# Kernel optimization log

Measured on AMD Instinct MI355X. Metric: run time of the kernel, lower is better.

## Reference

```python
import jax, jax.numpy as jnp
import numpy as np

P_SIZE = 5
NUM_HEAD = 8
GN_EPS = 1e-5
LRELU_SLOPE = 0.2


def conv1x1(w, x, b=None):
    # w: [out_c, in_c], x: [n, in_c, h, w]
    y = jnp.einsum('oc,nchw->nohw', w, x)
    if b is not None:
        y = y + b[None, :, None, None]
    return y


def bilinear_sample(feat, sx, sy):
    """grid_sample(mode='bilinear', padding_mode='zeros', align_corners=True).
    With align_corners=True the normalize/denormalize round-trip in
    deformation_grid/grid_sample is the identity, so sx,sy are raw pixel coords.
    feat: [n,c,H,W]; sx,sy: [n,P,H,W] -> out [n,c,P,H,W]."""
    n, c, H, W = feat.shape
    x0 = jnp.floor(sx)
    y0 = jnp.floor(sy)
    x1 = x0 + 1.0
    y1 = y0 + 1.0
    wx1 = sx - x0
    wx0 = 1.0 - wx1
    wy1 = sy - y0
    wy0 = 1.0 - wy1
    feat_flat = feat.reshape(n, c, H * W)

    def corner(xi, yi, wgt):
        valid = (xi >= 0) & (xi <= W - 1) & (yi >= 0) & (yi <= H - 1)
        xc = jnp.clip(xi, 0, W - 1).astype(jnp.int32)
        yc = jnp.clip(yi, 0, H - 1).astype(jnp.int32)
        idx = (yc * W + xc).reshape(n, -1)                      # [n, P*H*W]
        g = jnp.take_along_axis(feat_flat, idx[:, None, :], axis=2)  # [n,c,P*H*W]
        g = g.reshape(n, c, xi.shape[1], H, W)                  # [n,c,P,H,W]
        wm = (wgt * valid.astype(feat.dtype))[:, None]          # [n,1,P,H,W]
        return g * wm

    return (corner(x0, y0, wx0 * wy0) + corner(x1, y0, wx1 * wy0)
            + corner(x0, y1, wx0 * wy1) + corner(x1, y1, wx1 * wy1))


def sample_coords(deform_field, p_size):
    # deform_field: [n,2,h,w] -> absolute pixel coords sx, sy: [n, p^2, h, w]
    n, _, h, w = deform_field.shape
    padding = (p_size - 1) // 2
    shift = jnp.arange(p_size, dtype=deform_field.dtype) - padding
    shift_y, shift_x = jnp.meshgrid(shift, shift, indexing='ij')  # [p,p]
    shift_y = shift_y.reshape(-1, 1, 1)  # [p^2,1,1]
    shift_x = shift_x.reshape(-1, 1, 1)
    gy = jnp.arange(h, dtype=deform_field.dtype)[:, None]  # [h,1]
    gx = jnp.arange(w, dtype=deform_field.dtype)[None, :]  # [1,w]
    sx = gx[None] + shift_x + deform_field[:, None, 0]     # [n,p^2,h,w]
    sy = gy[None] + shift_y + deform_field[:, None, 1]
    return sx, sy


def setup_inputs() -> dict:
    key = jax.random.key(0)
    ks = jax.random.split(key, 12)
    n, c, h, w = 2, 128, 96, 96
    hid = 256
    s = 0.05
    return {
        'query': jax.random.normal(ks[0], (n, c, h, w), jnp.float32),
        'key': jax.random.normal(ks[1], (n, c, h, w), jnp.float32),
        'value': jax.random.normal(ks[2], (n, c, h, w), jnp.float32),
        'deform_field': jax.random.normal(ks[3], (n, 2, h, w), jnp.float32) * 2.0,
        'w_q': jax.random.normal(ks[4], (c, c), jnp.float32) * s,
        'w_k': jax.random.normal(ks[5], (c, c), jnp.float32) * s,
        'w_v': jax.random.normal(ks[6], (c, c), jnp.float32) * s,
        'w_fc': jax.random.normal(ks[7], (c, c), jnp.float32) * s,
        'mlp_w1': jax.random.normal(ks[8], (hid, c), jnp.float32) * s,
        'mlp_b1': jnp.zeros((hid,), jnp.float32),
        'mlp_w2': jax.random.normal(ks[9], (c, hid), jnp.float32) * s,
        'mlp_b2': jnp.zeros((c,), jnp.float32),
        'gn_gamma': jnp.ones((c,), jnp.float32),
        'gn_beta': jnp.zeros((c,), jnp.float32),
    }


def reference(query, key, value, deform_field, w_q, w_k, w_v, w_fc,
              mlp_w1, mlp_b1, mlp_w2, mlp_b2, gn_gamma, gn_beta):
    p2 = P_SIZE * P_SIZE
    n, c, h, w = query.shape
    d_k = c // NUM_HEAD

    q = conv1x1(w_q, query)   # [n,c,h,w]
    k = conv1x1(w_k, key)
    v = conv1x1(w_v, value)

    # deformable window sampling of keys/values
    sx, sy = sample_coords(deform_field, P_SIZE)      # [n,p^2,h,w]
    k_s = bilinear_sample(k, sx, sy)                  # [n,c,p^2,h,w]
    v_s = bilinear_sample(v, sx, sy)

    # split heads
    q = q.reshape(n, NUM_HEAD, d_k, h, w)
    k_s = k_s.reshape(n, NUM_HEAD, d_k, p2, h, w)
    v_s = v_s.reshape(n, NUM_HEAD, d_k, p2, h, w)

    scale = 1.0 / jnp.sqrt(jnp.asarray(d_k, q.dtype))
    attn = jnp.einsum('nedyx,nedpyx->neyxp', q * scale, k_s)   # [n,head,h,w,p^2]
    attn = jax.nn.softmax(attn, axis=-1)
    out = jnp.einsum('neyxp,nedpyx->nedyx', attn, v_s)          # [n,head,d_v,h,w]
    out = out.reshape(n, c, h, w)
    out = conv1x1(w_fc, out)

    # conv-MLP residual
    hdn = conv1x1(mlp_w1, out, mlp_b1)
    hdn = jnp.where(hdn >= 0, hdn, LRELU_SLOPE * hdn)
    out = out + conv1x1(mlp_w2, hdn, mlp_b2)

    # GroupNorm(1, feat_dim): normalize over (C,H,W) per sample, per-channel affine
    mean = jnp.mean(out, axis=(1, 2, 3), keepdims=True)
    var = jnp.mean(jnp.square(out - mean), axis=(1, 2, 3), keepdims=True)
    out = (out - mean) * jax.lax.rsqrt(var + GN_EPS)
    out = out * gn_gamma[None, :, None, None] + gn_beta[None, :, None, None]
    return out
```

## Files before the change

kernel.cpp:

```cpp
#include <hip/hip_runtime.h>
#include <cstddef>

constexpr int Cc = 128;
constexpr int Hh = 96;
constexpr int Ww = 96;
constexpr int HW = Hh * Ww;
constexpr int Nn = 2;

typedef __attribute__((ext_vector_type(2))) _Float16 f16x2;
typedef __attribute__((ext_vector_type(4))) _Float16 f16x4;
typedef __attribute__((ext_vector_type(8))) _Float16 f16x8;
typedef __attribute__((ext_vector_type(4))) float f32x4;

__device__ __forceinline__ float fdot2(f16x2 a, f16x2 b, float c) {
#if defined(__has_builtin) && __has_builtin(__builtin_amdgcn_fdot2)
    return __builtin_amdgcn_fdot2(a, b, c, false);
#else
    return (float)a[0] * (float)b[0] + (float)a[1] * (float)b[1] + c;
#endif
}

__global__ void __launch_bounds__(256)
wcvt_k(const float* __restrict__ wq, const float* __restrict__ wk,
       const float* __restrict__ wv, const float* __restrict__ wfc,
       const float* __restrict__ w1, const float* __restrict__ w2,
       _Float16* __restrict__ dst)
{
    const int h0 = (blockIdx.x * 256 + threadIdx.x) * 8;
    const float* src; int off, K;
    if (h0 < 16384)      { src = wq;  off = h0;          K = 128; }
    else if (h0 < 32768) { src = wk;  off = h0 - 16384;  K = 128; }
    else if (h0 < 49152) { src = wv;  off = h0 - 32768;  K = 128; }
    else if (h0 < 65536) { src = wfc; off = h0 - 49152;  K = 128; }
    else if (h0 < 98304) { src = w1;  off = h0 - 65536;  K = 128; }
    else                 { src = w2;  off = h0 - 98304;  K = 256; }
    const int fid  = off >> 3;
    const int lane = fid & 63;
    const int n16  = lane & 15, quad = lane >> 4;
    const int t2   = fid >> 6;
    const int kcN  = K / 32;
    const int kc   = t2 % kcN;
    const int mt   = t2 / kcN;
    const int row  = mt * 16 + n16;
    const int col  = kc * 32 + quad * 8;
    const float* s = src + (size_t)row * K + col;
    const float4 a = *(const float4*)s;
    const float4 b = *(const float4*)(s + 4);
    f16x8 h = {(_Float16)a.x, (_Float16)a.y, (_Float16)a.z, (_Float16)a.w,
               (_Float16)b.x, (_Float16)b.y, (_Float16)b.z, (_Float16)b.w};
    *(f16x8*)&dst[h0] = h;
}

__global__ void __launch_bounds__(128)
kv_k(const float* __restrict__ Xk, const float* __restrict__ Xv,
     const _Float16* __restrict__ w16,
     _Float16* __restrict__ k16, _Float16* __restrict__ v16)
{
    const int t  = blockIdx.y;
    const int p0 = blockIdx.x * 64;
    const int z  = blockIdx.z;
    const float* X = (t == 0) ? Xk : Xv;
    _Float16* Y    = (t == 0) ? k16 : v16;
    const _Float16* W = w16 + 16384 + (size_t)t * 16384;

    __shared__ _Float16 xl[128][72];
    const int tid = threadIdx.x;
    {
        const int px4 = (tid & 15) * 4, kg = tid >> 4;
        const float* Xz = X + (size_t)z * Cc * HW + p0 + px4;
#pragma unroll
        for (int kk = 0; kk < 16; ++kk) {
            const int k = kk * 8 + kg;
            float4 a = *(const float4*)&Xz[(size_t)k * HW];
            f16x4 h = {(_Float16)a.x, (_Float16)a.y, (_Float16)a.z, (_Float16)a.w};
            *(f16x4*)&xl[k][px4] = h;
        }
    }
    __syncthreads();

    const int w = tid >> 6, lane = tid & 63;
    const int n16 = lane & 15, quad = lane >> 4;
    const int pw = w * 32;

    f16x8 A[2][4];
#pragma unroll
    for (int mi = 0; mi < 2; ++mi) {
        const int px = pw + mi * 16 + n16;
#pragma unroll
        for (int kcid = 0; kcid < 4; ++kcid) {
            f16x8 av;
#pragma unroll
            for (int j = 0; j < 8; ++j) av[j] = xl[kcid * 32 + quad * 8 + j][px];
            A[mi][kcid] = av;
        }
    }

#pragma unroll
    for (int half = 0; half < 2; ++half) {
        const int oc0 = half * 64;
        f32x4 acc[2][4];
#pragma unroll
        for (int mi = 0; mi < 2; ++mi)
#pragma unroll
            for (int ni = 0; ni < 4; ++ni) acc[mi][ni] = (f32x4)0.f;

#pragma unroll
        for (int kcid = 0; kcid < 4; ++kcid) {
            f16x8 B[4];
#pragma unroll
            for (int ni = 0; ni < 4; ++ni)
                B[ni] = *(const f16x8*)&W[(((half * 4 + ni) * 4 + kcid) * 64 + lane) * 8];
#pragma unroll
            for (int mi = 0; mi < 2; ++mi)
#pragma unroll
                for (int ni = 0; ni < 4; ++ni)
                    acc[mi][ni] = __builtin_amdgcn_mfma_f32_16x16x32_f16(
                        A[mi][kcid], B[ni], acc[mi][ni], 0, 0, 0);
        }

#pragma unroll
        for (int mi = 0; mi < 2; ++mi)
#pragma unroll
            for (int r = 0; r < 4; ++r) {
                const int pix = p0 + pw + mi * 16 + quad * 4 + r;
                const size_t base = ((size_t)z * HW + pix) * Cc + oc0;
#pragma unroll
                for (int ni = 0; ni < 4; ++ni)
                    Y[base + ni * 16 + n16] = (_Float16)acc[mi][ni][r];
            }
    }
}

__global__ void __launch_bounds__(512)
qaf_k(const float* __restrict__ Xq, const _Float16* __restrict__ w16,
      const _Float16* __restrict__ k16, const _Float16* __restrict__ v16,
      const float* __restrict__ df, const float* __restrict__ b1,
      const float* __restrict__ b2, _Float16* __restrict__ y2,
      float* __restrict__ pb)
{
    __shared__ __align__(16) _Float16 xl[128][40];
    __shared__ __align__(16) _Float16 ql[32][136];
    __shared__ __align__(16) _Float16 y1l[32][136];
    __shared__ __align__(16) _Float16 hl[32][264];
    __shared__ float red[16];

    const int z  = blockIdx.z;
    const int bx = blockIdx.x;
    const int ti = (bx & 7) * 36 + (bx >> 3);
    const int p0 = ti * 32;
    const int tid = threadIdx.x, w = tid >> 6, lane = tid & 63;
    const int n16 = lane & 15, quad = lane >> 4;

    {
        const int px4 = (tid & 7) * 4, k0 = tid >> 3;
        const float* Xz = Xq + (size_t)z * Cc * HW + p0 + px4;
#pragma unroll
        for (int kk = 0; kk < 2; ++kk) {
            const int k = kk * 64 + k0;
            float4 a = *(const float4*)&Xz[(size_t)k * HW];
            f16x4 h4 = {(_Float16)a.x, (_Float16)a.y, (_Float16)a.z, (_Float16)a.w};
            *(f16x4*)&xl[k][px4] = h4;
        }
    }
    __syncthreads();

    {
        f32x4 qa[2];
        qa[0] = (f32x4)0.f; qa[1] = (f32x4)0.f;
#pragma unroll
        for (int kc = 0; kc < 4; ++kc) {
            f16x8 A[2];
#pragma unroll
            for (int mi = 0; mi < 2; ++mi) {
                f16x8 av;
#pragma unroll
                for (int j = 0; j < 8; ++j)
                    av[j] = xl[kc * 32 + quad * 8 + j][mi * 16 + n16];
                A[mi] = av;
            }
            const f16x8 B = *(const f16x8*)&w16[((w * 4 + kc) * 64 + lane) * 8];
#pragma unroll
            for (int mi = 0; mi < 2; ++mi)
                qa[mi] = __builtin_amdgcn_mfma_f32_16x16x32_f16(A[mi], B, qa[mi], 0, 0, 0);
        }
#pragma unroll
        for (int mi = 0; mi < 2; ++mi)
#pragma unroll
            for (int r = 0; r < 4; ++r)
                ql[mi * 16 + quad * 4 + r][w * 16 + n16] = (_Float16)qa[mi][r];
    }
    __syncthreads();

    {
        const int lpx = w * 4 + (lane >> 4);
        const int pix = p0 + lpx;
        const int y = pix / Ww, x = pix - y * Ww;
        const int co = n16 * 8;

        const float dx = df[((size_t)z * 2 + 0) * HW + pix];
        const float dy = df[((size_t)z * 2 + 1) * HW + pix];
        const float flx = floorf(dx), fly = floorf(dy);
        const int bxp = x - 2 + (int)flx;
        const int byp = y - 2 + (int)fly;
        const float wx1 = dx - flx, wx0 = 1.f - wx1;
        const float wy1 = dy - fly, wy0 = 1.f - wy1;
        const float s00 = wy0 * wx0 * 0.25f, s01 = wy0 * wx1 * 0.25f,
                    s10 = wy1 * wx0 * 0.25f, s11 = wy1 * wx1 * 0.25f;

        const f16x8 qv8 = *(const f16x8*)&ql[lpx][co];
        const f16x2 q0 = {qv8[0], qv8[1]}, q1 = {qv8[2], qv8[3]},
                    q2 = {qv8[4], qv8[5]}, q3 = {qv8[6], qv8[7]};

        const _Float16* kp = k16 + ((size_t)z * HW) * Cc + co;
        const _Float16* vp = v16 + ((size_t)z * HW) * Cc + co;

        const bool inb = (bxp >= 0) & (byp >= 0) & (bxp <= Ww - 6) & (byp <= Hh - 6);
        const int allin = __all(inb);

        float qk[36];
        if (allin) {
            const _Float16* kr = kp + (size_t)(byp * Ww + bxp) * Cc;
#pragma unroll
            for (int r = 0; r < 6; ++r) {
#pragma unroll
                for (int c = 0; c < 6; ++c) {
                    const f16x8 kv = *(const f16x8*)&kr[c * Cc];
                    f16x2 k0 = {kv[0], kv[1]}, k1 = {kv[2], kv[3]};
                    f16x2 k2 = {kv[4], kv[5]}, k3 = {kv[6], kv[7]};
                    float d = fdot2(q0, k0, 0.f);
                    d = fdot2(q1, k1, d);
                    d = fdot2(q2, k2, d);
                    d = fdot2(q3, k3, d);
                    qk[r * 6 + c] = d;
                }
                kr += Ww * Cc;
            }
        } else {
#pragma unroll
            for (int r = 0; r < 6; ++r) {
                const int yr = byp + r;
                const bool rv = (yr >= 0) & (yr < Hh);
                const int yc = min(max(yr, 0), Hh - 1);
                const _Float16* kr = kp + (size_t)(yc * Ww) * Cc;
#pragma unroll
                for (int c = 0; c < 6; ++c) {
                    const int xc = bxp + c;
                    const bool cv = rv & (xc >= 0) & (xc < Ww);
                    const int xcc = min(max(xc, 0), Ww - 1);
                    const f16x8 kv = *(const f16x8*)&kr[xcc * Cc];
                    f16x2 k0 = {kv[0], kv[1]}, k1 = {kv[2], kv[3]};
                    f16x2 k2 = {kv[4], kv[5]}, k3 = {kv[6], kv[7]};
                    float d = fdot2(q0, k0, 0.f);
                    d = fdot2(q1, k1, d);
                    d = fdot2(q2, k2, d);
                    d = fdot2(q3, k3, d);
                    qk[r * 6 + c] = cv ? d : 0.f;
                }
            }
        }

        float a[25];
#pragma unroll
        for (int py = 0; py < 5; ++py)
#pragma unroll
            for (int px = 0; px < 5; ++px) {
                float tv = s00 * qk[py * 6 + px];
                tv = fmaf(s01, qk[py * 6 + px + 1], tv);
                tv = fmaf(s10, qk[(py + 1) * 6 + px], tv);
                tv = fmaf(s11, qk[(py + 1) * 6 + px + 1], tv);
                a[py * 5 + px] = tv;
            }
#pragma unroll
        for (int i = 0; i < 25; ++i) a[i] += __shfl_xor(a[i], 1, 64);

        float mx = a[0];
#pragma unroll
        for (int i = 1; i < 25; ++i) mx = fmaxf(mx, a[i]);
        float ssum = 0.f;
#pragma unroll
        for (int i = 0; i < 25; ++i) { a[i] = __expf(a[i] - mx); ssum += a[i]; }
        const float inv = 1.f / ssum;

        float tmp[6][5];
#pragma unroll
        for (int r = 0; r < 6; ++r)
#pragma unroll
            for (int px = 0; px < 5; ++px) {
                float tv = 0.f;
                if (r < 5)  tv = a[r * 5 + px] * wy0;
                if (r >= 1) tv = fmaf(a[(r - 1) * 5 + px], wy1, tv);
                tmp[r][px] = tv;
            }
        float wsum[36];
#pragma unroll
        for (int r = 0; r < 6; ++r)
#pragma unroll
            for (int c = 0; c < 6; ++c) {
                float tv = 0.f;
                if (c < 5)  tv = tmp[r][c] * wx0;
                if (c >= 1) tv = fmaf(tmp[r][c - 1], wx1, tv);
                wsum[r * 6 + c] = tv;
            }

        float o[8] = {0.f, 0.f, 0.f, 0.f, 0.f, 0.f, 0.f, 0.f};
        if (allin) {
            const _Float16* vr = vp + (size_t)(byp * Ww + bxp) * Cc;
#pragma unroll
            for (int r = 0; r < 6; ++r) {
#pragma unroll
                for (int c = 0; c < 6; ++c) {
                    const f16x8 vv = *(const f16x8*)&vr[c * Cc];
                    const float wgt = wsum[r * 6 + c];
#pragma unroll
                    for (int j = 0; j < 8; ++j)
                        o[j] = fmaf(wgt, (float)vv[j], o[j]);
                }
                vr += Ww * Cc;
            }
        } else {
#pragma unroll
            for (int r = 0; r < 6; ++r) {
                const int yr = byp + r;
                const bool rv = (yr >= 0) & (yr < Hh);
                const int yc = min(max(yr, 0), Hh - 1);
                const _Float16* vr = vp + (size_t)(yc * Ww) * Cc;
#pragma unroll
                for (int c = 0; c < 6; ++c) {
                    const int xc = bxp + c;
                    const bool cv = rv & (xc >= 0) & (xc < Ww);
                    const int xcc = min(max(xc, 0), Ww - 1);
                    const f16x8 vv = *(const f16x8*)&vr[xcc * Cc];
                    const float wgt = cv ? wsum[r * 6 + c] : 0.f;
#pragma unroll
                    for (int j = 0; j < 8; ++j)
                        o[j] = fmaf(wgt, (float)vv[j], o[j]);
                }
            }
        }

        f16x8 ov;
#pragma unroll
        for (int j = 0; j < 8; ++j) ov[j] = (_Float16)(o[j] * inv);
        *(f16x8*)&ql[lpx][co] = ov;
    }
    __syncthreads();

    const _Float16* Wfc = w16 + 49152;
    const _Float16* W1  = w16 + 65536;
    const _Float16* W2  = w16 + 98304;

    f32x4 acc1[2];
    acc1[0] = (f32x4)0.f; acc1[1] = (f32x4)0.f;
#pragma unroll
    for (int kc = 0; kc < 4; ++kc) {
        f16x8 A[2];
#pragma unroll
        for (int mi = 0; mi < 2; ++mi)
            A[mi] = *(const f16x8*)&ql[mi * 16 + n16][kc * 32 + quad * 8];
        const f16x8 B = *(const f16x8*)&Wfc[((w * 4 + kc) * 64 + lane) * 8];
#pragma unroll
        for (int mi = 0; mi < 2; ++mi)
            acc1[mi] = __builtin_amdgcn_mfma_f32_16x16x32_f16(A[mi], B, acc1[mi], 0, 0, 0);
    }
#pragma unroll
    for (int mi = 0; mi < 2; ++mi)
#pragma unroll
        for (int r = 0; r < 4; ++r)
            y1l[mi * 16 + quad * 4 + r][w * 16 + n16] = (_Float16)acc1[mi][r];
    __syncthreads();

    {
        f32x4 acc2[2][2];
#pragma unroll
        for (int mi = 0; mi < 2; ++mi)
#pragma unroll
            for (int ni = 0; ni < 2; ++ni) acc2[mi][ni] = (f32x4)0.f;
#pragma unroll
        for (int kc = 0; kc < 4; ++kc) {
            f16x8 A[2];
#pragma unroll
            for (int mi = 0; mi < 2; ++mi)
                A[mi] = *(const f16x8*)&y1l[mi * 16 + n16][kc * 32 + quad * 8];
#pragma unroll
            for (int ni = 0; ni < 2; ++ni) {
                const f16x8 B = *(const f16x8*)&W1[(((w * 2 + ni) * 4 + kc) * 64 + lane) * 8];
#pragma unroll
                for (int mi = 0; mi < 2; ++mi)
                    acc2[mi][ni] = __builtin_amdgcn_mfma_f32_16x16x32_f16(
                        A[mi], B, acc2[mi][ni], 0, 0, 0);
            }
        }
        float b1v[2];
#pragma unroll
        for (int ni = 0; ni < 2; ++ni) b1v[ni] = b1[w * 32 + ni * 16 + n16];
#pragma unroll
        for (int mi = 0; mi < 2; ++mi)
#pragma unroll
            for (int ni = 0; ni < 2; ++ni)
#pragma unroll
                for (int r = 0; r < 4; ++r) {
                    float tv = acc2[mi][ni][r] + b1v[ni];
                    tv = tv >= 0.f ? tv : 0.2f * tv;
                    hl[mi * 16 + quad * 4 + r][w * 32 + ni * 16 + n16] = (_Float16)tv;
                }
    }
    __syncthreads();

    f32x4 acc3[2];
    acc3[0] = (f32x4)0.f; acc3[1] = (f32x4)0.f;
#pragma unroll
    for (int kc = 0; kc < 8; ++kc) {
        f16x8 A[2];
#pragma unroll
        for (int mi = 0; mi < 2; ++mi)
            A[mi] = *(const f16x8*)&hl[mi * 16 + n16][kc * 32 + quad * 8];
        const f16x8 B = *(const f16x8*)&W2[((w * 8 + kc) * 64 + lane) * 8];
#pragma unroll
        for (int mi = 0; mi < 2; ++mi)
            acc3[mi] = __builtin_amdgcn_mfma_f32_16x16x32_f16(A[mi], B, acc3[mi], 0, 0, 0);
    }

    const float b2v = b2[w * 16 + n16];
    float lsum = 0.f, lsq = 0.f;
#pragma unroll
    for (int mi = 0; mi < 2; ++mi)
#pragma unroll
        for (int r = 0; r < 4; ++r) {
            const int pix = p0 + mi * 16 + quad * 4 + r;
            const float tv = acc3[mi][r] + b2v + acc1[mi][r];
            lsum += tv; lsq += tv * tv;
            y2[((size_t)z * HW + pix) * Cc + w * 16 + n16] = (_Float16)tv;
        }

#pragma unroll
    for (int m = 1; m < 64; m <<= 1) {
        lsum += __shfl_xor(lsum, m, 64);
        lsq  += __shfl_xor(lsq,  m, 64);
    }
    if (lane == 0) { red[w * 2] = lsum; red[w * 2 + 1] = lsq; }
    __syncthreads();
    if (tid == 0) {
        float S = 0.f, Q = 0.f;
#pragma unroll
        for (int i = 0; i < 8; ++i) { S += red[i * 2]; Q += red[i * 2 + 1]; }
        const int bid = z * (HW / 32) + bx;
        pb[bid * 2 + 0] = S;
        pb[bid * 2 + 1] = Q;
    }
}

__global__ void __launch_bounds__(256)
gn_k(const _Float16* __restrict__ y2, const float* __restrict__ pb,
     const float* __restrict__ gamma, const float* __restrict__ beta,
     float* __restrict__ out, const int nPerZ)
{
    __shared__ float t[32][68];
    __shared__ float redm[8];
    __shared__ float stats[2];
    const int z = blockIdx.z, c0 = blockIdx.y * 32, p0 = blockIdx.x * 64;
    const int tid = threadIdx.x;

    {
        float s = 0.f, qq = 0.f;
        for (int p = tid; p < nPerZ; p += 256) {
            s  += pb[(z * nPerZ + p) * 2 + 0];
            qq += pb[(z * nPerZ + p) * 2 + 1];
        }
#pragma unroll
        for (int m = 1; m < 64; m <<= 1) {
            s  += __shfl_xor(s,  m, 64);
            qq += __shfl_xor(qq, m, 64);
        }
        if ((tid & 63) == 0) {
            redm[(tid >> 6) * 2]     = s;
            redm[(tid >> 6) * 2 + 1] = qq;
        }
    }
    {
        const int px = tid >> 2, cq = tid & 3;
        const f16x8 a = *(const f16x8*)&y2[((size_t)z * HW + p0 + px) * Cc + c0 + cq * 8];
#pragma unroll
        for (int j = 0; j < 8; ++j) t[cq * 8 + j][px] = (float)a[j];
    }
    __syncthreads();
    if (tid == 0) {
        const float invN = 1.f / (float)(Cc * HW);
        const float S = redm[0] + redm[2] + redm[4] + redm[6];
        const float Q = redm[1] + redm[3] + redm[5] + redm[7];
        const float mean = S * invN;
        const float var  = fmaf(-mean, mean, Q * invN);
        stats[0] = mean;
        stats[1] = rsqrtf(var + 1e-5f);
    }
    __syncthreads();
    {
        const float mean = stats[0], rs = stats[1];
        const int c = tid >> 3, pq = tid & 7;
        const float g = gamma[c0 + c] * rs, be = beta[c0 + c];
        float4 o1, o2;
        o1.x = fmaf(t[c][pq * 8 + 0] - mean, g, be);
        o1.y = fmaf(t[c][pq * 8 + 1] - mean, g, be);
        o1.z = fmaf(t[c][pq * 8 + 2] - mean, g, be);
        o1.w = fmaf(t[c][pq * 8 + 3] - mean, g, be);
        o2.x = fmaf(t[c][pq * 8 + 4] - mean, g, be);
        o2.y = fmaf(t[c][pq * 8 + 5] - mean, g, be);
        o2.z = fmaf(t[c][pq * 8 + 6] - mean, g, be);
        o2.w = fmaf(t[c][pq * 8 + 7] - mean, g, be);
        float* dst = &out[((size_t)z * Cc + c0 + c) * HW + p0 + pq * 8];
        *(float4*)dst = o1;
        *(float4*)(dst + 4) = o2;
    }
}

extern "C" void kernel_launch(void* const* d_in, const int* in_sizes, int n_in,
                              void* d_out, int out_size, void* d_ws, size_t ws_size,
                              hipStream_t stream)
{
    const float* query  = (const float*)d_in[0];
    const float* key    = (const float*)d_in[1];
    const float* value  = (const float*)d_in[2];
    const float* deform = (const float*)d_in[3];
    const float* w_q    = (const float*)d_in[4];
    const float* w_k    = (const float*)d_in[5];
    const float* w_v    = (const float*)d_in[6];
    const float* w_fc   = (const float*)d_in[7];
    const float* mlp_w1 = (const float*)d_in[8];
    const float* mlp_b1 = (const float*)d_in[9];
    const float* mlp_w2 = (const float*)d_in[10];
    const float* mlp_b2 = (const float*)d_in[11];
    const float* gn_g   = (const float*)d_in[12];
    const float* gn_b   = (const float*)d_in[13];
    float* out = (float*)d_out;

    char* wsb = (char*)d_ws;
    _Float16* w16 = (_Float16*)wsb;
    float* pb   = (float*)(wsb + 262144);
    _Float16* T = (_Float16*)(wsb + 524288);
    const size_t S16 = (size_t)Nn * HW * Cc;
    _Float16* k16  = T;
    _Float16* v16  = T + S16;
    _Float16* y2h  = T + 2 * S16;

    wcvt_k<<<dim3(64), dim3(256), 0, stream>>>(
        w_q, w_k, w_v, w_fc, mlp_w1, mlp_w2, w16);

    kv_k<<<dim3(HW / 64, 2, Nn), dim3(128), 0, stream>>>(
        key, value, w16, k16, v16);

    qaf_k<<<dim3(HW / 32, 1, Nn), dim3(512), 0, stream>>>(
        query, w16, k16, v16, deform, mlp_b1, mlp_b2, y2h, pb);

    gn_k<<<dim3(HW / 64, Cc / 32, Nn), dim3(256), 0, stream>>>(
        y2h, pb, gn_g, gn_b, out, HW / 32);
}
```

Baseline: 147.8 us.

## Fuse all stages into one cooperative persistent kernel with grid syncs

Replaces the four separate launches (weight conversion, K/V projection, attention+MLP, GroupNorm) with a single cooperative kernel that uses grid.sync between phases. The y2 tile stays in registers across the stats grid sync and is normalized and written directly, so the fp16 y2 round-trip through global memory and the separate gn pass go away. It also removes launch gaps between kernels. In exchange it adds grid-wide barrier costs, caps parallelism at the resident block count (256 or 512 blocks), and falls back to the old path if the cooperative launch fails.

```diff
diff --git a/kernel.cpp b/kernel.cpp
--- a/kernel.cpp
+++ b/kernel.cpp
@@ -1,5 +1,8 @@
 #include <hip/hip_runtime.h>
+#include <hip/hip_cooperative_groups.h>
 #include <cstddef>
+
+namespace cg = cooperative_groups;
 
 constexpr int Cc = 128;
 constexpr int Hh = 96;
@@ -20,13 +23,12 @@
 #endif
 }
 
-__global__ void __launch_bounds__(256)
-wcvt_k(const float* __restrict__ wq, const float* __restrict__ wk,
-       const float* __restrict__ wv, const float* __restrict__ wfc,
-       const float* __restrict__ w1, const float* __restrict__ w2,
-       _Float16* __restrict__ dst)
-{
-    const int h0 = (blockIdx.x * 256 + threadIdx.x) * 8;
+__device__ __forceinline__ void dev_wconv(
+    int h0, const float* __restrict__ wq, const float* __restrict__ wk,
+    const float* __restrict__ wv, const float* __restrict__ wfc,
+    const float* __restrict__ w1, const float* __restrict__ w2,
+    _Float16* __restrict__ dst)
+{
     const float* src; int off, K;
     if (h0 < 16384)      { src = wq;  off = h0;          K = 128; }
     else if (h0 < 32768) { src = wk;  off = h0 - 16384;  K = 128; }
@@ -51,105 +53,19 @@
     *(f16x8*)&dst[h0] = h;
 }
 
-__global__ void __launch_bounds__(128)
-kv_k(const float* __restrict__ Xk, const float* __restrict__ Xv,
-     const _Float16* __restrict__ w16,
-     _Float16* __restrict__ k16, _Float16* __restrict__ v16)
-{
-    const int t  = blockIdx.y;
-    const int p0 = blockIdx.x * 64;
-    const int z  = blockIdx.z;
-    const float* X = (t == 0) ? Xk : Xv;
-    _Float16* Y    = (t == 0) ? k16 : v16;
-    const _Float16* W = w16 + 16384 + (size_t)t * 16384;
-
-    __shared__ _Float16 xl[128][72];
-    const int tid = threadIdx.x;
-    {
-        const int px4 = (tid & 15) * 4, kg = tid >> 4;
-        const float* Xz = X + (size_t)z * Cc * HW + p0 + px4;
-#pragma unroll
-        for (int kk = 0; kk < 16; ++kk) {
-            const int k = kk * 8 + kg;
-            float4 a = *(const float4*)&Xz[(size_t)k * HW];
-            f16x4 h = {(_Float16)a.x, (_Float16)a.y, (_Float16)a.z, (_Float16)a.w};
-            *(f16x4*)&xl[k][px4] = h;
-        }
-    }
-    __syncthreads();
-
+__device__ __forceinline__ f16x8 att_mlp_tile(
+    const int z, const int p0, const int tid,
+    const float* __restrict__ Xq, const _Float16* __restrict__ w16,
+    const _Float16* __restrict__ k16, const _Float16* __restrict__ v16,
+    const float* __restrict__ df, const float* __restrict__ b1,
+    const float* __restrict__ b2,
+    _Float16 (*xl)[40], _Float16 (*ql)[136], _Float16 (*y1l)[136],
+    _Float16 (*hl)[264], float* red, float* __restrict__ pbOut)
+{
     const int w = tid >> 6, lane = tid & 63;
     const int n16 = lane & 15, quad = lane >> 4;
-    const int pw = w * 32;
-
-    f16x8 A[2][4];
-#pragma unroll
-    for (int mi = 0; mi < 2; ++mi) {
-        const int px = pw + mi * 16 + n16;
-#pragma unroll
-        for (int kcid = 0; kcid < 4; ++kcid) {
-            f16x8 av;
-#pragma unroll
-            for (int j = 0; j < 8; ++j) av[j] = xl[kcid * 32 + quad * 8 + j][px];
-            A[mi][kcid] = av;
-        }
-    }
-
-#pragma unroll
-    for (int half = 0; half < 2; ++half) {
-        const int oc0 = half * 64;
-        f32x4 acc[2][4];
-#pragma unroll
-        for (int mi = 0; mi < 2; ++mi)
-#pragma unroll
-            for (int ni = 0; ni < 4; ++ni) acc[mi][ni] = (f32x4)0.f;
-
-#pragma unroll
-        for (int kcid = 0; kcid < 4; ++kcid) {
-            f16x8 B[4];
-#pragma unroll
-            for (int ni = 0; ni < 4; ++ni)
-                B[ni] = *(const f16x8*)&W[(((half * 4 + ni) * 4 + kcid) * 64 + lane) * 8];
-#pragma unroll
-            for (int mi = 0; mi < 2; ++mi)
-#pragma unroll
-                for (int ni = 0; ni < 4; ++ni)
-                    acc[mi][ni] = __builtin_amdgcn_mfma_f32_16x16x32_f16(
-                        A[mi][kcid], B[ni], acc[mi][ni], 0, 0, 0);
-        }
-
-#pragma unroll
-        for (int mi = 0; mi < 2; ++mi)
-#pragma unroll
-            for (int r = 0; r < 4; ++r) {
-                const int pix = p0 + pw + mi * 16 + quad * 4 + r;
-                const size_t base = ((size_t)z * HW + pix) * Cc + oc0;
-#pragma unroll
-                for (int ni = 0; ni < 4; ++ni)
-                    Y[base + ni * 16 + n16] = (_Float16)acc[mi][ni][r];
-            }
-    }
-}
-
-__global__ void __launch_bounds__(512)
-qaf_k(const float* __restrict__ Xq, const _Float16* __restrict__ w16,
-      const _Float16* __restrict__ k16, const _Float16* __restrict__ v16,
-      const float* __restrict__ df, const float* __restrict__ b1,
-      const float* __restrict__ b2, _Float16* __restrict__ y2,
-      float* __restrict__ pb)
-{
-    __shared__ __align__(16) _Float16 xl[128][40];
-    __shared__ __align__(16) _Float16 ql[32][136];
-    __shared__ __align__(16) _Float16 y1l[32][136];
-    __shared__ __align__(16) _Float16 hl[32][264];
-    __shared__ float red[16];
-
-    const int z  = blockIdx.z;
-    const int bx = blockIdx.x;
-    const int ti = (bx & 7) * 36 + (bx >> 3);
-    const int p0 = ti * 32;
-    const int tid = threadIdx.x, w = tid >> 6, lane = tid & 63;
-    const int n16 = lane & 15, quad = lane >> 4;
+
+    __syncthreads();
 
     {
         const int px4 = (tid & 7) * 4, k0 = tid >> 3;
@@ -421,15 +337,15 @@
     }
 
     const float b2v = b2[w * 16 + n16];
+    f16x8 y2s;
     float lsum = 0.f, lsq = 0.f;
 #pragma unroll
     for (int mi = 0; mi < 2; ++mi)
 #pragma unroll
         for (int r = 0; r < 4; ++r) {
-            const int pix = p0 + mi * 16 + quad * 4 + r;
             const float tv = acc3[mi][r] + b2v + acc1[mi][r];
             lsum += tv; lsq += tv * tv;
-            y2[((size_t)z * HW + pix) * Cc + w * 16 + n16] = (_Float16)tv;
+            y2s[mi * 4 + r] = (_Float16)tv;
         }
 
 #pragma unroll
@@ -443,10 +359,318 @@
         float S = 0.f, Q = 0.f;
 #pragma unroll
         for (int i = 0; i < 8; ++i) { S += red[i * 2]; Q += red[i * 2 + 1]; }
-        const int bid = z * (HW / 32) + bx;
-        pb[bid * 2 + 0] = S;
-        pb[bid * 2 + 1] = Q;
-    }
+        pbOut[0] = S;
+        pbOut[1] = Q;
+    }
+    return y2s;
+}
+
+__device__ __forceinline__ void gn_write_tile(
+    const int tile, const f16x8 y2s, const int tid,
+    _Float16 (*t16)[40], const float* stats, const float gv, const float bv,
+    float* __restrict__ out)
+{
+    const int z = tile / 288, p0 = (tile % 288) * 32;
+    const int w = tid >> 6, lane = tid & 63;
+    const int n16 = lane & 15, quad = lane >> 4;
+
+    __syncthreads();
+    const int c = w * 16 + n16;
+    f16x4 lo = {y2s[0], y2s[1], y2s[2], y2s[3]};
+    f16x4 hi = {y2s[4], y2s[5], y2s[6], y2s[7]};
+    *(f16x4*)&t16[c][quad * 4] = lo;
+    *(f16x4*)&t16[c][16 + quad * 4] = hi;
+    __syncthreads();
+
+    const int cc = tid >> 2, pq = tid & 3;
+    const f16x8 vv = *(const f16x8*)&t16[cc][pq * 8];
+    const float mean = stats[z * 2], rs = stats[z * 2 + 1];
+    const float gg = gv * rs;
+    float4 o1, o2;
+    o1.x = fmaf((float)vv[0] - mean, gg, bv);
+    o1.y = fmaf((float)vv[1] - mean, gg, bv);
+    o1.z = fmaf((float)vv[2] - mean, gg, bv);
+    o1.w = fmaf((float)vv[3] - mean, gg, bv);
+    o2.x = fmaf((float)vv[4] - mean, gg, bv);
+    o2.y = fmaf((float)vv[5] - mean, gg, bv);
+    o2.z = fmaf((float)vv[6] - mean, gg, bv);
+    o2.w = fmaf((float)vv[7] - mean, gg, bv);
+    float* dst = &out[((size_t)z * Cc + cc) * HW + p0 + pq * 8];
+    *(float4*)dst = o1;
+    *(float4*)(dst + 4) = o2;
+}
+
+__global__ void __launch_bounds__(512)
+mono_k(const float* __restrict__ q_in, const float* __restrict__ k_in,
+       const float* __restrict__ v_in, const float* __restrict__ df,
+       const float* __restrict__ wq, const float* __restrict__ wk,
+       const float* __restrict__ wv, const float* __restrict__ wfc,
+       const float* __restrict__ w1, const float* __restrict__ w2,
+       const float* __restrict__ b1, const float* __restrict__ b2,
+       const float* __restrict__ gamma, const float* __restrict__ beta,
+       _Float16* __restrict__ w16, _Float16* __restrict__ k16,
+       _Float16* __restrict__ v16, float* __restrict__ pb,
+       float* __restrict__ out)
+{
+    __shared__ __align__(16) char smem[44544];
+    __shared__ float red[16];
+    __shared__ float red2[32];
+    __shared__ float stats[4];
+    auto xl  = (_Float16 (*)[40]) smem;
+    auto ql  = (_Float16 (*)[136])(smem + 10240);
+    auto y1l = (_Float16 (*)[136])(smem + 18944);
+    auto hl  = (_Float16 (*)[264])(smem + 27648);
+    auto xk  = (_Float16 (*)[72]) smem;
+    auto xv  = (_Float16 (*)[72])(smem + 18432);
+    auto t16 = (_Float16 (*)[40]) smem;
+
+    const int bid = blockIdx.x, tid = threadIdx.x, nb = gridDim.x;
+    cg::grid_group grid = cg::this_grid();
+
+    {
+        const int gtid = bid * 512 + tid;
+        if (gtid < 16384) dev_wconv(gtid * 8, wq, wk, wv, wfc, w1, w2, w16);
+    }
+    grid.sync();
+
+    for (int u = bid; u < 288; u += nb) {
+        __syncthreads();
+        const int z = u / 144, p0 = (u % 144) * 64;
+        const int g = tid >> 8, gt = tid & 255;
+        _Float16 (*xs)[72] = g ? xv : xk;
+        const float* X = g ? v_in : k_in;
+        _Float16* Y = g ? v16 : k16;
+        const _Float16* W = w16 + 16384 + g * 16384;
+        {
+            const int px4 = (gt & 15) * 4, kg = gt >> 4;
+            const float* Xz = X + (size_t)z * Cc * HW + p0 + px4;
+#pragma unroll
+            for (int kk = 0; kk < 8; ++kk) {
+                const int k = kk * 16 + kg;
+                float4 a = *(const float4*)&Xz[(size_t)k * HW];
+                f16x4 h = {(_Float16)a.x, (_Float16)a.y, (_Float16)a.z, (_Float16)a.w};
+                *(f16x4*)&xs[k][px4] = h;
+            }
+        }
+        __syncthreads();
+        {
+            const int wvid = gt >> 6, lane = gt & 63;
+            const int n16 = lane & 15, quad = lane >> 4;
+            const int pw = (wvid & 1) * 32, half = wvid >> 1, oc0 = half * 64;
+            f16x8 A[2][4];
+#pragma unroll
+            for (int mi = 0; mi < 2; ++mi) {
+                const int px = pw + mi * 16 + n16;
+#pragma unroll
+                for (int kcid = 0; kcid < 4; ++kcid) {
+                    f16x8 av;
+#pragma unroll
+                    for (int j = 0; j < 8; ++j) av[j] = xs[kcid * 32 + quad * 8 + j][px];
+                    A[mi][kcid] = av;
+                }
+            }
+            f32x4 acc[2][4];
+#pragma unroll
+            for (int mi = 0; mi < 2; ++mi)
+#pragma unroll
+                for (int ni = 0; ni < 4; ++ni) acc[mi][ni] = (f32x4)0.f;
+#pragma unroll
+            for (int kcid = 0; kcid < 4; ++kcid) {
+                f16x8 B[4];
+#pragma unroll
+                for (int ni = 0; ni < 4; ++ni)
+                    B[ni] = *(const f16x8*)&W[(((half * 4 + ni) * 4 + kcid) * 64 + lane) * 8];
+#pragma unroll
+                for (int mi = 0; mi < 2; ++mi)
+#pragma unroll
+                    for (int ni = 0; ni < 4; ++ni)
+                        acc[mi][ni] = __builtin_amdgcn_mfma_f32_16x16x32_f16(
+                            A[mi][kcid], B[ni], acc[mi][ni], 0, 0, 0);
+            }
+#pragma unroll
+            for (int mi = 0; mi < 2; ++mi)
+#pragma unroll
+                for (int r = 0; r < 4; ++r) {
+                    const int pix = p0 + pw + mi * 16 + quad * 4 + r;
+                    const size_t base = ((size_t)z * HW + pix) * Cc + oc0;
+#pragma unroll
+                    for (int ni = 0; ni < 4; ++ni)
+                        Y[base + ni * 16 + n16] = (_Float16)acc[mi][ni][r];
+                }
+        }
+    }
+    grid.sync();
+
+    const int xcd = bid & 7, slot = bid >> 3, step = nb >> 3;
+    int t0 = -1, t1 = -1, t2 = -1;
+    { const int lin = slot;            if (lin < 72) t0 = xcd * 72 + lin; }
+    { const int lin = slot + step;     if (lin < 72) t1 = xcd * 72 + lin; }
+    { const int lin = slot + 2 * step; if (lin < 72) t2 = xcd * 72 + lin; }
+    f16x8 y2s0{}, y2s1{}, y2s2{};
+    if (t0 >= 0) y2s0 = att_mlp_tile(t0 / 288, (t0 % 288) * 32, tid, q_in, w16,
+                                     k16, v16, df, b1, b2, xl, ql, y1l, hl, red, &pb[t0 * 2]);
+    if (t1 >= 0) y2s1 = att_mlp_tile(t1 / 288, (t1 % 288) * 32, tid, q_in, w16,
+                                     k16, v16, df, b1, b2, xl, ql, y1l, hl, red, &pb[t1 * 2]);
+    if (t2 >= 0) y2s2 = att_mlp_tile(t2 / 288, (t2 % 288) * 32, tid, q_in, w16,
+                                     k16, v16, df, b1, b2, xl, ql, y1l, hl, red, &pb[t2 * 2]);
+    grid.sync();
+
+    {
+        float s0 = 0.f, q0 = 0.f, s1 = 0.f, q1 = 0.f;
+        for (int i = tid; i < 288; i += 512) {
+            s0 += pb[i * 2];          q0 += pb[i * 2 + 1];
+            s1 += pb[(i + 288) * 2];  q1 += pb[(i + 288) * 2 + 1];
+        }
+#pragma unroll
+        for (int m = 1; m < 64; m <<= 1) {
+            s0 += __shfl_xor(s0, m, 64); q0 += __shfl_xor(q0, m, 64);
+            s1 += __shfl_xor(s1, m, 64); q1 += __shfl_xor(q1, m, 64);
+        }
+        const int w = tid >> 6, lane = tid & 63;
+        if (lane == 0) {
+            red2[w * 4] = s0; red2[w * 4 + 1] = q0;
+            red2[w * 4 + 2] = s1; red2[w * 4 + 3] = q1;
+        }
+        __syncthreads();
+        if (tid == 0) {
+            float S0 = 0.f, Q0 = 0.f, S1 = 0.f, Q1 = 0.f;
+#pragma unroll
+            for (int i = 0; i < 8; ++i) {
+                S0 += red2[i * 4];     Q0 += red2[i * 4 + 1];
+                S1 += red2[i * 4 + 2]; Q1 += red2[i * 4 + 3];
+            }
+            const float invN = 1.f / (float)(Cc * HW);
+            const float m0 = S0 * invN, v0 = fmaf(-m0, m0, Q0 * invN);
+            const float m1 = S1 * invN, v1 = fmaf(-m1, m1, Q1 * invN);
+            stats[0] = m0; stats[1] = rsqrtf(v0 + 1e-5f);
+            stats[2] = m1; stats[3] = rsqrtf(v1 + 1e-5f);
+        }
+        __syncthreads();
+    }
+    const float gv = gamma[tid >> 2], bv = beta[tid >> 2];
+    if (t0 >= 0) gn_write_tile(t0, y2s0, tid, t16, stats, gv, bv, out);
+    if (t1 >= 0) gn_write_tile(t1, y2s1, tid, t16, stats, gv, bv, out);
+    if (t2 >= 0) gn_write_tile(t2, y2s2, tid, t16, stats, gv, bv, out);
+}
+
+__global__ void __launch_bounds__(256)
+wcvt_k(const float* __restrict__ wq, const float* __restrict__ wk,
+       const float* __restrict__ wv, const float* __restrict__ wfc,
+       const float* __restrict__ w1, const float* __restrict__ w2,
+       _Float16* __restrict__ dst)
+{
+    dev_wconv((blockIdx.x * 256 + threadIdx.x) * 8, wq, wk, wv, wfc, w1, w2, dst);
+}
+
+__global__ void __launch_bounds__(128)
+kv_k(const float* __restrict__ Xk, const float* __restrict__ Xv,
+     const _Float16* __restrict__ w16,
+     _Float16* __restrict__ k16, _Float16* __restrict__ v16)
+{
+    const int t  = blockIdx.y;
+    const int p0 = blockIdx.x * 64;
+    const int z  = blockIdx.z;
+    const float* X = (t == 0) ? Xk : Xv;
+    _Float16* Y    = (t == 0) ? k16 : v16;
+    const _Float16* W = w16 + 16384 + (size_t)t * 16384;
+
+    __shared__ _Float16 xl[128][72];
+    const int tid = threadIdx.x;
+    {
+        const int px4 = (tid & 15) * 4, kg = tid >> 4;
+        const float* Xz = X + (size_t)z * Cc * HW + p0 + px4;
+#pragma unroll
+        for (int kk = 0; kk < 16; ++kk) {
+            const int k = kk * 8 + kg;
+            float4 a = *(const float4*)&Xz[(size_t)k * HW];
+            f16x4 h = {(_Float16)a.x, (_Float16)a.y, (_Float16)a.z, (_Float16)a.w};
+            *(f16x4*)&xl[k][px4] = h;
+        }
+    }
+    __syncthreads();
+
+    const int w = tid >> 6, lane = tid & 63;
+    const int n16 = lane & 15, quad = lane >> 4;
+    const int pw = w * 32;
+
+    f16x8 A[2][4];
+#pragma unroll
+    for (int mi = 0; mi < 2; ++mi) {
+        const int px = pw + mi * 16 + n16;
+#pragma unroll
+        for (int kcid = 0; kcid < 4; ++kcid) {
+            f16x8 av;
+#pragma unroll
+            for (int j = 0; j < 8; ++j) av[j] = xl[kcid * 32 + quad * 8 + j][px];
+            A[mi][kcid] = av;
+        }
+    }
+
+#pragma unroll
+    for (int half = 0; half < 2; ++half) {
+        const int oc0 = half * 64;
+        f32x4 acc[2][4];
+#pragma unroll
+        for (int mi = 0; mi < 2; ++mi)
+#pragma unroll
+            for (int ni = 0; ni < 4; ++ni) acc[mi][ni] = (f32x4)0.f;
+
+#pragma unroll
+        for (int kcid = 0; kcid < 4; ++kcid) {
+            f16x8 B[4];
+#pragma unroll
+            for (int ni = 0; ni < 4; ++ni)
+                B[ni] = *(const f16x8*)&W[(((half * 4 + ni) * 4 + kcid) * 64 + lane) * 8];
+#pragma unroll
+            for (int mi = 0; mi < 2; ++mi)
+#pragma unroll
+                for (int ni = 0; ni < 4; ++ni)
+                    acc[mi][ni] = __builtin_amdgcn_mfma_f32_16x16x32_f16(
+                        A[mi][kcid], B[ni], acc[mi][ni], 0, 0, 0);
+        }
+
+#pragma unroll
+        for (int mi = 0; mi < 2; ++mi)
+#pragma unroll
+            for (int r = 0; r < 4; ++r) {
+                const int pix = p0 + pw + mi * 16 + quad * 4 + r;
+                const size_t base = ((size_t)z * HW + pix) * Cc + oc0;
+#pragma unroll
+                for (int ni = 0; ni < 4; ++ni)
+                    Y[base + ni * 16 + n16] = (_Float16)acc[mi][ni][r];
+            }
+    }
+}
+
+__global__ void __launch_bounds__(512)
+qaf_k(const float* __restrict__ Xq, const _Float16* __restrict__ w16,
+      const _Float16* __restrict__ k16, const _Float16* __restrict__ v16,
+      const float* __restrict__ df, const float* __restrict__ b1,
+      const float* __restrict__ b2, _Float16* __restrict__ y2,
+      float* __restrict__ pb)
+{
+    __shared__ __align__(16) _Float16 xl[128][40];
+    __shared__ __align__(16) _Float16 ql[32][136];
+    __shared__ __align__(16) _Float16 y1l[32][136];
+    __shared__ __align__(16) _Float16 hl[32][264];
+    __shared__ float red[16];
+
+    const int z  = blockIdx.z;
+    const int bx = blockIdx.x;
+    const int ti = (bx & 7) * 36 + (bx >> 3);
+    const int p0 = ti * 32;
+    const int tid = threadIdx.x, w = tid >> 6, lane = tid & 63;
+    const int n16 = lane & 15, quad = lane >> 4;
+
+    f16x8 y2s = att_mlp_tile(z, p0, tid, Xq, w16, k16, v16, df, b1, b2,
+                             xl, ql, y1l, hl, red, &pb[((size_t)z * 288 + bx) * 2]);
+#pragma unroll
+    for (int mi = 0; mi < 2; ++mi)
+#pragma unroll
+        for (int r = 0; r < 4; ++r) {
+            const int pix = p0 + mi * 16 + quad * 4 + r;
+            y2[((size_t)z * HW + pix) * Cc + w * 16 + n16] = y2s[mi * 4 + r];
+        }
 }
 
 __global__ void __launch_bounds__(256)
@@ -459,7 +683,6 @@
     __shared__ float stats[2];
     const int z = blockIdx.z, c0 = blockIdx.y * 32, p0 = blockIdx.x * 64;
     const int tid = threadIdx.x;
-
     {
         float s = 0.f, qq = 0.f;
         for (int p = tid; p < nPerZ; p += 256) {
@@ -541,15 +764,28 @@
     _Float16* v16  = T + S16;
     _Float16* y2h  = T + 2 * S16;
 
-    wcvt_k<<<dim3(64), dim3(256), 0, stream>>>(
-        w_q, w_k, w_v, w_fc, mlp_w1, mlp_w2, w16);
-
-    kv_k<<<dim3(HW / 64, 2, Nn), dim3(128), 0, stream>>>(
-        key, value, w16, k16, v16);
-
-    qaf_k<<<dim3(HW / 32, 1, Nn), dim3(512), 0, stream>>>(
-        query, w16, k16, v16, deform, mlp_b1, mlp_b2, y2h, pb);
-
-    gn_k<<<dim3(HW / 64, Cc / 32, Nn), dim3(256), 0, stream>>>(
-        y2h, pb, gn_g, gn_b, out, HW / 32);
-}
+    int occ = 0;
+    hipError_t oe = hipOccupancyMaxActiveBlocksPerMultiprocessor(&occ, mono_k, 512, 0);
+    const int nb = (oe == hipSuccess && occ >= 2) ? 512 : 256;
+
+    void* args[] = {
+        (void*)&query, (void*)&key, (void*)&value, (void*)&deform,
+        (void*)&w_q, (void*)&w_k, (void*)&w_v, (void*)&w_fc,
+        (void*)&mlp_w1, (void*)&mlp_w2, (void*)&mlp_b1, (void*)&mlp_b2,
+        (void*)&gn_g, (void*)&gn_b,
+        (void*)&w16, (void*)&k16, (void*)&v16, (void*)&pb, (void*)&out
+    };
+    hipError_t e = hipLaunchCooperativeKernel(mono_k, dim3(nb), dim3(512),
+                                              args, 0u, stream);
+    if (e != hipSuccess) {
+        (void)hipGetLastError();
+        wcvt_k<<<dim3(64), dim3(256), 0, stream>>>(
+            w_q, w_k, w_v, w_fc, mlp_w1, mlp_w2, w16);
+        kv_k<<<dim3(HW / 64, 2, Nn), dim3(128), 0, stream>>>(
+            key, value, w16, k16, v16);
+        qaf_k<<<dim3(HW / 32, 1, Nn), dim3(512), 0, stream>>>(
+            query, w16, k16, v16, deform, mlp_b1, mlp_b2, y2h, pb);
+        gn_k<<<dim3(HW / 64, Cc / 32, Nn), dim3(256), 0, stream>>>(
+            y2h, pb, gn_g, gn_b, out, HW / 32);
+    }
+}
```

Result: slower. 248.1 us (+67.9%).
